# Kernel tuning notes

Measured on AMD Instinct MI355X. Metric: run time of the kernel, lower is better.

Reference implementation:

```python
import jax, jax.numpy as jnp
import numpy as np

N_NODES = 100000
N_EDGES = 1600000
NFEAT, NHID, NCLASS = 512, 128, 40


def setup_inputs() -> dict:
    key = jax.random.key(0)
    ks = jax.random.split(key, 8)
    features = jax.random.normal(ks[0], (N_NODES, NFEAT), dtype=jnp.float32)
    edge_src = jax.random.randint(ks[1], (N_EDGES,), 0, N_NODES, dtype=jnp.int32)
    edge_dst = jax.random.randint(ks[2], (N_EDGES,), 0, N_NODES, dtype=jnp.int32)
    edge_weight = jax.random.uniform(ks[3], (N_EDGES,), dtype=jnp.float32)
    W1 = jax.random.normal(ks[4], (NFEAT, NHID), dtype=jnp.float32) * (1.0 / np.sqrt(NFEAT))
    b1 = jnp.zeros((NHID,), dtype=jnp.float32)
    W2 = jax.random.normal(ks[5], (NHID, NCLASS), dtype=jnp.float32) * (1.0 / np.sqrt(NHID))
    b2 = jnp.zeros((NCLASS,), dtype=jnp.float32)
    return {"features": features, "edge_src": edge_src, "edge_dst": edge_dst,
            "edge_weight": edge_weight, "W1": W1, "b1": b1, "W2": W2, "b2": b2}


def _gcn_conv(x, W, b, edge_src, edge_dst, edge_weight, num_nodes):
    # GCNconv: adj @ (x @ W) + b, adj given as weighted edge list (spmm).
    h = x @ W                                   # [N, out]
    msgs = edge_weight[:, None] * h[edge_src]   # [E, out] gather + scale
    agg = jax.ops.segment_sum(msgs, edge_dst, num_segments=num_nodes)  # [N, out]
    return agg + b


def reference(features, edge_src, edge_dst, edge_weight, W1, b1, W2, b2):
    x = _gcn_conv(features, W1, b1, edge_src, edge_dst, edge_weight, N_NODES)
    x = jax.nn.relu(x)
    # dropout is identity in eval mode (deterministic reference)
    x = _gcn_conv(x, W2, b2, edge_src, edge_dst, edge_weight, N_NODES)
    return jax.nn.log_softmax(x, axis=1)
```

## Files before the change

kernel.cpp:

```cpp
#include <hip/hip_runtime.h>
#include <hip/hip_bf16.h>
#include <math.h>

#define N_NODES 100000
#define N_EDGES 1600000
#define NFEAT 512
#define NHID 128
#define NCLASS 40

#define SCAN_TILE 1024
#define SCAN_NB ((N_NODES + SCAN_TILE - 1) / SCAN_TILE)

#define BSH 8
#define BNODES (1 << BSH)
#define NBUCK ((N_NODES + BNODES - 1) / BNODES)

#define PCHUNK 4096
#define PEPT 16
#define PNB ((N_EDGES + PCHUNK - 1) / PCHUNK)

typedef short bf16x8 __attribute__((ext_vector_type(8)));
typedef float f32x4 __attribute__((ext_vector_type(4)));

static __device__ __forceinline__ unsigned short f32_to_bf16(float f) {
    unsigned int u = __float_as_uint(f);
    unsigned int r = u + 0x7FFFu + ((u >> 16) & 1u);
    return (unsigned short)(r >> 16);
}
static __device__ __forceinline__ float bf16_to_f32(unsigned short h) {
    return __uint_as_float(((unsigned int)h) << 16);
}

__global__ __launch_bounds__(256) void transpose_w1_kernel(
    const float* __restrict__ W1, unsigned short* __restrict__ Wt)
{
    int tid = blockIdx.x * 256 + threadIdx.x;
    int n = tid >> 9;
    int k = tid & 511;
    Wt[tid] = f32_to_bf16(W1[k * NHID + n]);
}

__global__ __launch_bounds__(256) void gemm1_mfma_kernel(
    const float* __restrict__ A,
    const unsigned short* __restrict__ Wt,
    unsigned short* __restrict__ h1b,
    int M)
{
    __shared__ unsigned short cstage[4][32 * 130];

    const int tid = threadIdx.x;
    const int w = tid >> 6;
    const int lane = tid & 63;
    const int lr = lane & 15;
    const int quad = lane >> 4;
    const int m0 = blockIdx.x * 128 + w * 32;

    f32x4 acc[2][8];
    #pragma unroll
    for (int rt = 0; rt < 2; rt++)
        #pragma unroll
        for (int ct = 0; ct < 8; ct++)
            acc[rt][ct] = (f32x4){0.f, 0.f, 0.f, 0.f};

    int r0 = m0 + lr;
    int r1 = m0 + 16 + lr;
    int r0c = r0 < M ? r0 : M - 1;
    int r1c = r1 < M ? r1 : M - 1;
    const float* a0p = A + (size_t)r0c * NFEAT + quad * 8;
    const float* a1p = A + (size_t)r1c * NFEAT + quad * 8;
    const unsigned short* bp = Wt + (size_t)lr * NFEAT + quad * 8;

    #pragma unroll 2
    for (int k0 = 0; k0 < NFEAT; k0 += 32) {
        float4 a0a = *(const float4*)(a0p + k0);
        float4 a0b = *(const float4*)(a0p + k0 + 4);
        float4 a1a = *(const float4*)(a1p + k0);
        float4 a1b = *(const float4*)(a1p + k0 + 4);

        bf16x8 fb[8];
        #pragma unroll
        for (int ct = 0; ct < 8; ct++)
            fb[ct] = *(const bf16x8*)(bp + (size_t)ct * 16 * NFEAT + k0);

        bf16x8 fa0, fa1;
        fa0[0] = (short)f32_to_bf16(a0a.x); fa0[1] = (short)f32_to_bf16(a0a.y);
        fa0[2] = (short)f32_to_bf16(a0a.z); fa0[3] = (short)f32_to_bf16(a0a.w);
        fa0[4] = (short)f32_to_bf16(a0b.x); fa0[5] = (short)f32_to_bf16(a0b.y);
        fa0[6] = (short)f32_to_bf16(a0b.z); fa0[7] = (short)f32_to_bf16(a0b.w);
        fa1[0] = (short)f32_to_bf16(a1a.x); fa1[1] = (short)f32_to_bf16(a1a.y);
        fa1[2] = (short)f32_to_bf16(a1a.z); fa1[3] = (short)f32_to_bf16(a1a.w);
        fa1[4] = (short)f32_to_bf16(a1b.x); fa1[5] = (short)f32_to_bf16(a1b.y);
        fa1[6] = (short)f32_to_bf16(a1b.z); fa1[7] = (short)f32_to_bf16(a1b.w);

        #pragma unroll
        for (int ct = 0; ct < 8; ct++) {
            acc[0][ct] = __builtin_amdgcn_mfma_f32_16x16x32_bf16(fa0, fb[ct], acc[0][ct], 0, 0, 0);
            acc[1][ct] = __builtin_amdgcn_mfma_f32_16x16x32_bf16(fa1, fb[ct], acc[1][ct], 0, 0, 0);
        }
    }

    unsigned short* st = cstage[w];
    #pragma unroll
    for (int rt = 0; rt < 2; rt++)
        #pragma unroll
        for (int ct = 0; ct < 8; ct++)
            #pragma unroll
            for (int i = 0; i < 4; i++) {
                int row = rt * 16 + quad * 4 + i;
                int col = ct * 16 + lr;
                st[row * 130 + col] = f32_to_bf16(acc[rt][ct][i]);
            }

    #pragma unroll
    for (int g = 0; g < 8; g++) {
        int row = g * 4 + (lane >> 4);
        int c8 = lane & 15;
        const unsigned short* rp = &st[row * 130 + c8 * 8];
        uint4 v = *(const uint4*)rp;
        int gr = m0 + row;
        if (gr < M)
            *(uint4*)&h1b[(size_t)gr * NHID + c8 * 8] = v;
    }
}

__global__ __launch_bounds__(256) void hist_kernel(
    const int* __restrict__ dst, int* __restrict__ counts, int E)
{
    int e = blockIdx.x * 256 + threadIdx.x;
    if (e < E) atomicAdd(&counts[dst[e]], 1);
}

__global__ __launch_bounds__(256) void scan_partials_kernel(
    const int* __restrict__ counts, int* __restrict__ partials, int N)
{
    __shared__ int sh[256];
    const int t = threadIdx.x;
    const int base = blockIdx.x * SCAN_TILE + t * 4;
    int s = 0;
    #pragma unroll
    for (int j = 0; j < 4; j++) {
        int i = base + j;
        if (i < N) s += counts[i];
    }
    sh[t] = s;
    __syncthreads();
    #pragma unroll
    for (int off = 128; off > 0; off >>= 1) {
        if (t < off) sh[t] += sh[t + off];
        __syncthreads();
    }
    if (t == 0) partials[blockIdx.x] = sh[0];
}

__global__ __launch_bounds__(128) void scan_offsets_kernel(
    const int* __restrict__ partials, int* __restrict__ bofs,
    int* __restrict__ offsets, int N)
{
    __shared__ int sh[128];
    const int t = threadIdx.x;
    int v = (t < SCAN_NB) ? partials[t] : 0;
    sh[t] = v;
    __syncthreads();
    #pragma unroll
    for (int off = 1; off < 128; off <<= 1) {
        int u = (t >= off) ? sh[t - off] : 0;
        __syncthreads();
        sh[t] += u;
        __syncthreads();
    }
    if (t < SCAN_NB) bofs[t] = sh[t] - v;
    if (t == 127) offsets[N] = sh[127];
}

__global__ __launch_bounds__(256) void scan_final_kernel(
    const int* __restrict__ counts, const int* __restrict__ bofs,
    int* __restrict__ offsets, int N)
{
    __shared__ int sh[256];
    const int t = threadIdx.x;
    const int base = blockIdx.x * SCAN_TILE + t * 4;
    int c[4] = {0, 0, 0, 0};
    #pragma unroll
    for (int j = 0; j < 4; j++) {
        int i = base + j;
        if (i < N) c[j] = counts[i];
    }
    int s = c[0] + c[1] + c[2] + c[3];
    sh[t] = s;
    __syncthreads();
    #pragma unroll
    for (int off = 1; off < 256; off <<= 1) {
        int u = (t >= off) ? sh[t - off] : 0;
        __syncthreads();
        sh[t] += u;
        __syncthreads();
    }
    int run = bofs[blockIdx.x] + sh[t] - s;
    #pragma unroll
    for (int j = 0; j < 4; j++) {
        int i = base + j;
        if (i < N) {
            offsets[i] = run;
            run += c[j];
        }
    }
}

__global__ __launch_bounds__(256) void bucket_init_kernel(
    const int* __restrict__ offsets, int* __restrict__ bcursor, int N)
{
    int b = blockIdx.x * 256 + threadIdx.x;
    if (b < NBUCK) {
        int nb = b << BSH;
        bcursor[b] = offsets[nb < N ? nb : N];
    }
}

__global__ __launch_bounds__(256) void partition_kernel(
    const int* __restrict__ src, const int* __restrict__ dst,
    const float* __restrict__ w, int* __restrict__ bcursor,
    int2* __restrict__ sortedA, int E)
{
    __shared__ int hist[NBUCK];
    __shared__ int bbase[NBUCK];
    const int t = threadIdx.x;
    const int c0 = blockIdx.x * PCHUNK;

    for (int j = t; j < NBUCK; j += 256) hist[j] = 0;
    __syncthreads();

    int  myb[PEPT];
    int2 myv[PEPT];
    #pragma unroll
    for (int i = 0; i < PEPT; i++) {
        int e = c0 + t + i * 256;
        if (e < E) {
            int d = dst[e];
            myb[i] = d >> BSH;
            myv[i] = make_int2(src[e] | ((d & (BNODES - 1)) << 17),
                               __float_as_int(w[e]));
            atomicAdd(&hist[myb[i]], 1);
        } else {
            myb[i] = -1;
        }
    }
    __syncthreads();

    for (int j = t; j < NBUCK; j += 256) {
        int c = hist[j];
        bbase[j] = c ? atomicAdd(&bcursor[j], c) : 0;
    }
    __syncthreads();

    #pragma unroll
    for (int i = 0; i < PEPT; i++) {
        if (myb[i] >= 0) {
            int p = atomicAdd(&bbase[myb[i]], 1);
            sortedA[p] = myv[i];
        }
    }
}

__global__ __launch_bounds__(256) void bucket_sort_kernel(
    const int2* __restrict__ sortedA, const int* __restrict__ offsets,
    int2* __restrict__ sortedB, int N)
{
    __shared__ int lcur[BNODES];
    const int b = blockIdx.x;
    const int t = threadIdx.x;
    const int nb = b << BSH;
    const int nn = min(BNODES, N - nb);
    if (t < nn) lcur[t] = offsets[nb + t];
    __syncthreads();
    const int beg = offsets[nb];
    const int end = offsets[nb + nn < N ? nb + nn : N];
    for (int e = beg + t; e < end; e += 256) {
        int2 v = sortedA[e];
        int dlow = (v.x >> 17) & (BNODES - 1);
        int s = v.x & 0x1FFFF;
        int p = atomicAdd(&lcur[dlow], 1);
        sortedB[p] = make_int2(s, v.y);
    }
}

__global__ __launch_bounds__(256) void seg_agg1_kernel(
    const int2* __restrict__ sorted, const int* __restrict__ offsets,
    const unsigned short* __restrict__ h1b, const float* __restrict__ b1,
    float* __restrict__ x, int N)
{
    const int tid = threadIdx.x;
    const int lane = tid & 31;
    const int node = blockIdx.x * 8 + (tid >> 5);
    if (node >= N) return;
    const int beg = offsets[node];
    const int end = offsets[node + 1];
    float4 acc = {0.f, 0.f, 0.f, 0.f};
    for (int c = beg; c < end; c += 32) {
        int m = end - c;
        if (m > 32) m = 32;
        int s = 0, wb = 0;
        if (lane < m) { int2 sw = sorted[c + lane]; s = sw.x; wb = sw.y; }
        for (int j = 0; j < m; j++) {
            int sj = __shfl(s, j, 32);
            float wj = __int_as_float(__shfl(wb, j, 32));
            ushort4 hv = *(const ushort4*)(h1b + (size_t)sj * NHID + lane * 4);
            acc.x = fmaf(wj, bf16_to_f32(hv.x), acc.x);
            acc.y = fmaf(wj, bf16_to_f32(hv.y), acc.y);
            acc.z = fmaf(wj, bf16_to_f32(hv.z), acc.z);
            acc.w = fmaf(wj, bf16_to_f32(hv.w), acc.w);
        }
    }
    float4 bb = *(const float4*)&b1[lane * 4];
    acc.x = fmaxf(acc.x + bb.x, 0.f);
    acc.y = fmaxf(acc.y + bb.y, 0.f);
    acc.z = fmaxf(acc.z + bb.z, 0.f);
    acc.w = fmaxf(acc.w + bb.w, 0.f);
    *(float4*)&x[(size_t)node * NHID + lane * 4] = acc;
}

__global__ __launch_bounds__(256) void gemm2_kernel(
    const float* __restrict__ x, const float* __restrict__ W2,
    float* __restrict__ h2, int M)
{
    __shared__ float xs[32][128];
    __shared__ float Wt[40][132];

    const int tid = threadIdx.x;
    const int m0 = blockIdx.x * 32;

    #pragma unroll
    for (int i = 0; i < 4; i++) {
        int v = tid + i * 256;
        int row = v >> 5;
        int c4 = (v & 31) * 4;
        *(float4*)&xs[row][c4] = *(const float4*)&x[(size_t)(m0 + row) * NHID + c4];
    }
    #pragma unroll
    for (int i = 0; i < 20; i++) {
        int v = tid + i * 256;
        int k = v / 40;
        int c = v - k * 40;
        Wt[c][k] = W2[v];
    }
    __syncthreads();

    #pragma unroll
    for (int i = 0; i < 5; i++) {
        int o = tid + i * 256;
        int row = o / 40;
        int col = o - row * 40;
        float s = 0.f;
        #pragma unroll
        for (int k4 = 0; k4 < 32; k4++) {
            float4 x4 = *(float4*)&xs[row][k4 * 4];
            float4 w4 = *(float4*)&Wt[col][k4 * 4];
            s = fmaf(x4.x, w4.x, s);
            s = fmaf(x4.y, w4.y, s);
            s = fmaf(x4.z, w4.z, s);
            s = fmaf(x4.w, w4.w, s);
        }
        h2[(size_t)(m0 + row) * NCLASS + col] = s;
    }
}

__global__ __launch_bounds__(256) void seg_agg2_kernel(
    const int2* __restrict__ sorted, const int* __restrict__ offsets,
    const float* __restrict__ h2, const float* __restrict__ b2,
    float* __restrict__ out, int N)
{
    const int tid = threadIdx.x;
    const int lane = tid & 15;
    const int node = blockIdx.x * 16 + (tid >> 4);
    if (node >= N) return;
    const int beg = offsets[node];
    const int end = offsets[node + 1];
    float4 acc = {0.f, 0.f, 0.f, 0.f};
    for (int c = beg; c < end; c += 16) {
        int m = end - c;
        if (m > 16) m = 16;
        int s = 0, wb = 0;
        if (lane < m) { int2 sw = sorted[c + lane]; s = sw.x; wb = sw.y; }
        for (int j = 0; j < m; j++) {
            int sj = __shfl(s, j, 16);
            float wj = __int_as_float(__shfl(wb, j, 16));
            if (lane < 10) {
                float4 v = *(const float4*)&h2[(size_t)sj * NCLASS + lane * 4];
                acc.x = fmaf(wj, v.x, acc.x);
                acc.y = fmaf(wj, v.y, acc.y);
                acc.z = fmaf(wj, v.z, acc.z);
                acc.w = fmaf(wj, v.w, acc.w);
            }
        }
    }
    float mx;
    if (lane < 10) {
        float4 bb = *(const float4*)&b2[lane * 4];
        acc.x += bb.x; acc.y += bb.y; acc.z += bb.z; acc.w += bb.w;
        mx = fmaxf(fmaxf(acc.x, acc.y), fmaxf(acc.z, acc.w));
    } else {
        mx = -INFINITY;
    }
    #pragma unroll
    for (int o = 8; o > 0; o >>= 1) mx = fmaxf(mx, __shfl_xor(mx, o, 16));
    float sm = 0.f;
    if (lane < 10)
        sm = expf(acc.x - mx) + expf(acc.y - mx) + expf(acc.z - mx) + expf(acc.w - mx);
    #pragma unroll
    for (int o = 8; o > 0; o >>= 1) sm += __shfl_xor(sm, o, 16);
    if (lane < 10) {
        float l = mx + logf(sm);
        float4 o4 = {acc.x - l, acc.y - l, acc.z - l, acc.w - l};
        *(float4*)&out[(size_t)node * NCLASS + lane * 4] = o4;
    }
}

extern "C" void kernel_launch(void* const* d_in, const int* in_sizes, int n_in,
                              void* d_out, int out_size, void* d_ws, size_t ws_size,
                              hipStream_t stream) {
    const float* features = (const float*)d_in[0];
    const int* edge_src   = (const int*)d_in[1];
    const int* edge_dst   = (const int*)d_in[2];
    const float* edge_w   = (const float*)d_in[3];
    const float* W1       = (const float*)d_in[4];
    const float* b1       = (const float*)d_in[5];
    const float* W2       = (const float*)d_in[6];
    const float* b2       = (const float*)d_in[7];
    float* out = (float*)d_out;

    char* base = (char*)d_ws;
    float*          x        = (float*)base;
    unsigned short* h1b      = (unsigned short*)(base + 51200000);
    unsigned short* Wt       = (unsigned short*)(base + 76800000);
    int2*           sortedB  = (int2*)(base + 76931072);
    int*            offsets  = (int*)(base + 89731072);
    int*            counts   = (int*)(base + 90131080);
    int*            partials = (int*)(base + 90531080);
    int*            bofs     = (int*)(base + 90531472);
    int*            bcursor  = (int*)(base + 90532000);
    int2*           sortedA  = (int2*)(base + 90540000);
    float*          h2       = (float*)h1b;

    hipMemsetAsync(counts, 0, N_NODES * sizeof(int), stream);

    hist_kernel<<<(N_EDGES + 255) / 256, 256, 0, stream>>>(edge_dst, counts, N_EDGES);
    scan_partials_kernel<<<SCAN_NB, 256, 0, stream>>>(counts, partials, N_NODES);
    scan_offsets_kernel<<<1, 128, 0, stream>>>(partials, bofs, offsets, N_NODES);
    scan_final_kernel<<<SCAN_NB, 256, 0, stream>>>(counts, bofs, offsets, N_NODES);
    bucket_init_kernel<<<(NBUCK + 255) / 256, 256, 0, stream>>>(offsets, bcursor, N_NODES);
    partition_kernel<<<PNB, 256, 0, stream>>>(
        edge_src, edge_dst, edge_w, bcursor, sortedA, N_EDGES);
    bucket_sort_kernel<<<NBUCK, 256, 0, stream>>>(sortedA, offsets, sortedB, N_NODES);

    transpose_w1_kernel<<<(NFEAT * NHID) / 256, 256, 0, stream>>>(W1, Wt);
    gemm1_mfma_kernel<<<(N_NODES + 127) / 128, 256, 0, stream>>>(features, Wt, h1b, N_NODES);

    seg_agg1_kernel<<<(N_NODES + 7) / 8, 256, 0, stream>>>(
        sortedB, offsets, h1b, b1, x, N_NODES);

    gemm2_kernel<<<(N_NODES + 31) / 32, 256, 0, stream>>>(x, W2, h2, N_NODES);

    seg_agg2_kernel<<<(N_NODES + 15) / 16, 256, 0, stream>>>(
        sortedB, offsets, h2, b2, out, N_NODES);
}
```

Measured before the change: 645.4 us.

## Replace per-node CSR sort with bucket partition and LDS-atomic aggregation fused with gemm2

Drops the full per-node histogram, three-pass scan and second-level bucket sort. Edges are now only partitioned into 128-node buckets. Each bucket block accumulates messages into shared memory with LDS float atomics, then fuses bias, ReLU and the second GEMM (layer 1), or bias and log-softmax (layer 2). The W1 transpose is folded into the histogram launch, removing several launches and a global round trip of the intermediate x. The cost is LDS atomic contention, nondeterministic summation order, and W2 rounded to bf16.

```diff
diff --git a/kernel.cpp b/kernel.cpp
--- a/kernel.cpp
+++ b/kernel.cpp
@@ -8,10 +8,7 @@
 #define NHID 128
 #define NCLASS 40
 
-#define SCAN_TILE 1024
-#define SCAN_NB ((N_NODES + SCAN_TILE - 1) / SCAN_TILE)
-
-#define BSH 8
+#define BSH 7
 #define BNODES (1 << BSH)
 #define NBUCK ((N_NODES + BNODES - 1) / BNODES)
 
@@ -31,189 +28,57 @@
     return __uint_as_float(((unsigned int)h) << 16);
 }
 
-__global__ __launch_bounds__(256) void transpose_w1_kernel(
-    const float* __restrict__ W1, unsigned short* __restrict__ Wt)
-{
-    int tid = blockIdx.x * 256 + threadIdx.x;
-    int n = tid >> 9;
-    int k = tid & 511;
-    Wt[tid] = f32_to_bf16(W1[k * NHID + n]);
-}
-
-__global__ __launch_bounds__(256) void gemm1_mfma_kernel(
-    const float* __restrict__ A,
-    const unsigned short* __restrict__ Wt,
-    unsigned short* __restrict__ h1b,
-    int M)
-{
-    __shared__ unsigned short cstage[4][32 * 130];
-
-    const int tid = threadIdx.x;
-    const int w = tid >> 6;
-    const int lane = tid & 63;
-    const int lr = lane & 15;
-    const int quad = lane >> 4;
-    const int m0 = blockIdx.x * 128 + w * 32;
-
-    f32x4 acc[2][8];
-    #pragma unroll
-    for (int rt = 0; rt < 2; rt++)
-        #pragma unroll
-        for (int ct = 0; ct < 8; ct++)
-            acc[rt][ct] = (f32x4){0.f, 0.f, 0.f, 0.f};
-
-    int r0 = m0 + lr;
-    int r1 = m0 + 16 + lr;
-    int r0c = r0 < M ? r0 : M - 1;
-    int r1c = r1 < M ? r1 : M - 1;
-    const float* a0p = A + (size_t)r0c * NFEAT + quad * 8;
-    const float* a1p = A + (size_t)r1c * NFEAT + quad * 8;
-    const unsigned short* bp = Wt + (size_t)lr * NFEAT + quad * 8;
-
-    #pragma unroll 2
-    for (int k0 = 0; k0 < NFEAT; k0 += 32) {
-        float4 a0a = *(const float4*)(a0p + k0);
-        float4 a0b = *(const float4*)(a0p + k0 + 4);
-        float4 a1a = *(const float4*)(a1p + k0);
-        float4 a1b = *(const float4*)(a1p + k0 + 4);
-
-        bf16x8 fb[8];
-        #pragma unroll
-        for (int ct = 0; ct < 8; ct++)
-            fb[ct] = *(const bf16x8*)(bp + (size_t)ct * 16 * NFEAT + k0);
-
-        bf16x8 fa0, fa1;
-        fa0[0] = (short)f32_to_bf16(a0a.x); fa0[1] = (short)f32_to_bf16(a0a.y);
-        fa0[2] = (short)f32_to_bf16(a0a.z); fa0[3] = (short)f32_to_bf16(a0a.w);
-        fa0[4] = (short)f32_to_bf16(a0b.x); fa0[5] = (short)f32_to_bf16(a0b.y);
-        fa0[6] = (short)f32_to_bf16(a0b.z); fa0[7] = (short)f32_to_bf16(a0b.w);
-        fa1[0] = (short)f32_to_bf16(a1a.x); fa1[1] = (short)f32_to_bf16(a1a.y);
-        fa1[2] = (short)f32_to_bf16(a1a.z); fa1[3] = (short)f32_to_bf16(a1a.w);
-        fa1[4] = (short)f32_to_bf16(a1b.x); fa1[5] = (short)f32_to_bf16(a1b.y);
-        fa1[6] = (short)f32_to_bf16(a1b.z); fa1[7] = (short)f32_to_bf16(a1b.w);
-
-        #pragma unroll
-        for (int ct = 0; ct < 8; ct++) {
-            acc[0][ct] = __builtin_amdgcn_mfma_f32_16x16x32_bf16(fa0, fb[ct], acc[0][ct], 0, 0, 0);
-            acc[1][ct] = __builtin_amdgcn_mfma_f32_16x16x32_bf16(fa1, fb[ct], acc[1][ct], 0, 0, 0);
-        }
-    }
-
-    unsigned short* st = cstage[w];
-    #pragma unroll
-    for (int rt = 0; rt < 2; rt++)
-        #pragma unroll
-        for (int ct = 0; ct < 8; ct++)
-            #pragma unroll
-            for (int i = 0; i < 4; i++) {
-                int row = rt * 16 + quad * 4 + i;
-                int col = ct * 16 + lr;
-                st[row * 130 + col] = f32_to_bf16(acc[rt][ct][i]);
-            }
-
-    #pragma unroll
-    for (int g = 0; g < 8; g++) {
-        int row = g * 4 + (lane >> 4);
-        int c8 = lane & 15;
-        const unsigned short* rp = &st[row * 130 + c8 * 8];
-        uint4 v = *(const uint4*)rp;
-        int gr = m0 + row;
-        if (gr < M)
-            *(uint4*)&h1b[(size_t)gr * NHID + c8 * 8] = v;
-    }
-}
-
-__global__ __launch_bounds__(256) void hist_kernel(
-    const int* __restrict__ dst, int* __restrict__ counts, int E)
-{
-    int e = blockIdx.x * 256 + threadIdx.x;
-    if (e < E) atomicAdd(&counts[dst[e]], 1);
-}
-
-__global__ __launch_bounds__(256) void scan_partials_kernel(
-    const int* __restrict__ counts, int* __restrict__ partials, int N)
-{
-    __shared__ int sh[256];
+__global__ __launch_bounds__(256) void bucket_hist_transpose_kernel(
+    const int* __restrict__ dst, int* __restrict__ histG,
+    const float* __restrict__ W1, unsigned short* __restrict__ Wt, int E)
+{
+    const int blk = blockIdx.x;
+    if (blk >= PNB) {
+        int tid2 = (blk - PNB) * 256 + threadIdx.x;
+        int n = tid2 >> 9;
+        int k = tid2 & 511;
+        Wt[tid2] = f32_to_bf16(W1[k * NHID + n]);
+        return;
+    }
+    __shared__ int hl[NBUCK];
     const int t = threadIdx.x;
-    const int base = blockIdx.x * SCAN_TILE + t * 4;
-    int s = 0;
-    #pragma unroll
-    for (int j = 0; j < 4; j++) {
-        int i = base + j;
-        if (i < N) s += counts[i];
-    }
-    sh[t] = s;
-    __syncthreads();
-    #pragma unroll
-    for (int off = 128; off > 0; off >>= 1) {
-        if (t < off) sh[t] += sh[t + off];
-        __syncthreads();
-    }
-    if (t == 0) partials[blockIdx.x] = sh[0];
-}
-
-__global__ __launch_bounds__(128) void scan_offsets_kernel(
-    const int* __restrict__ partials, int* __restrict__ bofs,
-    int* __restrict__ offsets, int N)
-{
-    __shared__ int sh[128];
+    for (int j = t; j < NBUCK; j += 256) hl[j] = 0;
+    __syncthreads();
+    const int c0 = blk * PCHUNK;
+    #pragma unroll
+    for (int i = 0; i < PEPT; i++) {
+        int e = c0 + t + i * 256;
+        if (e < E) atomicAdd(&hl[dst[e] >> BSH], 1);
+    }
+    __syncthreads();
+    for (int j = t; j < NBUCK; j += 256) {
+        int c = hl[j];
+        if (c) atomicAdd(&histG[j * 16], c);
+    }
+}
+
+__global__ __launch_bounds__(1024) void bucket_scan_kernel(
+    const int* __restrict__ histG, int* __restrict__ bofs,
+    int* __restrict__ bcursor)
+{
+    __shared__ int sh[1024];
     const int t = threadIdx.x;
-    int v = (t < SCAN_NB) ? partials[t] : 0;
+    int v = (t < NBUCK) ? histG[t * 16] : 0;
     sh[t] = v;
     __syncthreads();
     #pragma unroll
-    for (int off = 1; off < 128; off <<= 1) {
+    for (int off = 1; off < 1024; off <<= 1) {
         int u = (t >= off) ? sh[t - off] : 0;
         __syncthreads();
         sh[t] += u;
         __syncthreads();
     }
-    if (t < SCAN_NB) bofs[t] = sh[t] - v;
-    if (t == 127) offsets[N] = sh[127];
-}
-
-__global__ __launch_bounds__(256) void scan_final_kernel(
-    const int* __restrict__ counts, const int* __restrict__ bofs,
-    int* __restrict__ offsets, int N)
-{
-    __shared__ int sh[256];
-    const int t = threadIdx.x;
-    const int base = blockIdx.x * SCAN_TILE + t * 4;
-    int c[4] = {0, 0, 0, 0};
-    #pragma unroll
-    for (int j = 0; j < 4; j++) {
-        int i = base + j;
-        if (i < N) c[j] = counts[i];
-    }
-    int s = c[0] + c[1] + c[2] + c[3];
-    sh[t] = s;
-    __syncthreads();
-    #pragma unroll
-    for (int off = 1; off < 256; off <<= 1) {
-        int u = (t >= off) ? sh[t - off] : 0;
-        __syncthreads();
-        sh[t] += u;
-        __syncthreads();
-    }
-    int run = bofs[blockIdx.x] + sh[t] - s;
-    #pragma unroll
-    for (int j = 0; j < 4; j++) {
-        int i = base + j;
-        if (i < N) {
-            offsets[i] = run;
-            run += c[j];
-        }
-    }
-}
-
-__global__ __launch_bounds__(256) void bucket_init_kernel(
-    const int* __restrict__ offsets, int* __restrict__ bcursor, int N)
-{
-    int b = blockIdx.x * 256 + threadIdx.x;
-    if (b < NBUCK) {
-        int nb = b << BSH;
-        bcursor[b] = offsets[nb < N ? nb : N];
-    }
+    if (t < NBUCK) {
+        int excl = sh[t] - v;
+        bofs[t] = excl;
+        bcursor[t] = excl;
+    }
+    if (t == NBUCK - 1) bofs[NBUCK] = sh[t];
 }
 
 __global__ __launch_bounds__(256) void partition_kernel(
@@ -261,156 +126,256 @@
     }
 }
 
-__global__ __launch_bounds__(256) void bucket_sort_kernel(
-    const int2* __restrict__ sortedA, const int* __restrict__ offsets,
-    int2* __restrict__ sortedB, int N)
-{
-    __shared__ int lcur[BNODES];
+__global__ __launch_bounds__(256) void gemm1_mfma_kernel(
+    const float* __restrict__ A,
+    const unsigned short* __restrict__ Wt,
+    unsigned short* __restrict__ h1b,
+    int M)
+{
+    __shared__ unsigned short cstage[4][32 * 130];
+
+    const int tid = threadIdx.x;
+    const int w = tid >> 6;
+    const int lane = tid & 63;
+    const int lr = lane & 15;
+    const int quad = lane >> 4;
+    const int m0 = blockIdx.x * 128 + w * 32;
+
+    f32x4 acc[2][8];
+    #pragma unroll
+    for (int rt = 0; rt < 2; rt++)
+        #pragma unroll
+        for (int ct = 0; ct < 8; ct++)
+            acc[rt][ct] = (f32x4){0.f, 0.f, 0.f, 0.f};
+
+    int r0 = m0 + lr;
+    int r1 = m0 + 16 + lr;
+    int r0c = r0 < M ? r0 : M - 1;
+    int r1c = r1 < M ? r1 : M - 1;
+    const float* a0p = A + (size_t)r0c * NFEAT + quad * 8;
+    const float* a1p = A + (size_t)r1c * NFEAT + quad * 8;
+    const unsigned short* bp = Wt + (size_t)lr * NFEAT + quad * 8;
+
+    #pragma unroll 2
+    for (int k0 = 0; k0 < NFEAT; k0 += 32) {
+        float4 a0a = *(const float4*)(a0p + k0);
+        float4 a0b = *(const float4*)(a0p + k0 + 4);
+        float4 a1a = *(const float4*)(a1p + k0);
+        float4 a1b = *(const float4*)(a1p + k0 + 4);
+
+        bf16x8 fb[8];
+        #pragma unroll
+        for (int ct = 0; ct < 8; ct++)
+            fb[ct] = *(const bf16x8*)(bp + (size_t)ct * 16 * NFEAT + k0);
+
+        bf16x8 fa0, fa1;
+        fa0[0] = (short)f32_to_bf16(a0a.x); fa0[1] = (short)f32_to_bf16(a0a.y);
+        fa0[2] = (short)f32_to_bf16(a0a.z); fa0[3] = (short)f32_to_bf16(a0a.w);
+        fa0[4] = (short)f32_to_bf16(a0b.x); fa0[5] = (short)f32_to_bf16(a0b.y);
+        fa0[6] = (short)f32_to_bf16(a0b.z); fa0[7] = (short)f32_to_bf16(a0b.w);
+        fa1[0] = (short)f32_to_bf16(a1a.x); fa1[1] = (short)f32_to_bf16(a1a.y);
+        fa1[2] = (short)f32_to_bf16(a1a.z); fa1[3] = (short)f32_to_bf16(a1a.w);
+        fa1[4] = (short)f32_to_bf16(a1b.x); fa1[5] = (short)f32_to_bf16(a1b.y);
+        fa1[6] = (short)f32_to_bf16(a1b.z); fa1[7] = (short)f32_to_bf16(a1b.w);
+
+        #pragma unroll
+        for (int ct = 0; ct < 8; ct++) {
+            acc[0][ct] = __builtin_amdgcn_mfma_f32_16x16x32_bf16(fa0, fb[ct], acc[0][ct], 0, 0, 0);
+            acc[1][ct] = __builtin_amdgcn_mfma_f32_16x16x32_bf16(fa1, fb[ct], acc[1][ct], 0, 0, 0);
+        }
+    }
+
+    unsigned short* st = cstage[w];
+    #pragma unroll
+    for (int rt = 0; rt < 2; rt++)
+        #pragma unroll
+        for (int ct = 0; ct < 8; ct++)
+            #pragma unroll
+            for (int i = 0; i < 4; i++) {
+                int row = rt * 16 + quad * 4 + i;
+                int col = ct * 16 + lr;
+                st[row * 130 + col] = f32_to_bf16(acc[rt][ct][i]);
+            }
+
+    #pragma unroll
+    for (int g = 0; g < 8; g++) {
+        int row = g * 4 + (lane >> 4);
+        int c8 = lane & 15;
+        const unsigned short* rp = &st[row * 130 + c8 * 8];
+        uint4 v = *(const uint4*)rp;
+        int gr = m0 + row;
+        if (gr < M)
+            *(uint4*)&h1b[(size_t)gr * NHID + c8 * 8] = v;
+    }
+}
+
+__global__ __launch_bounds__(256) void agg1_gemm2_kernel(
+    const int2* __restrict__ sortedA, const int* __restrict__ bofs,
+    const unsigned short* __restrict__ h1b, const float* __restrict__ b1,
+    const float* __restrict__ W2, float* __restrict__ h2, int N)
+{
+    __shared__ __align__(16) float accf[128 * 132];
+    __shared__ __align__(16) unsigned short wt2[40 * 132];
+    __shared__ float b1p[128];
+
+    const int tid = threadIdx.x;
     const int b = blockIdx.x;
-    const int t = threadIdx.x;
-    const int nb = b << BSH;
-    const int nn = min(BNODES, N - nb);
-    if (t < nn) lcur[t] = offsets[nb + t];
-    __syncthreads();
-    const int beg = offsets[nb];
-    const int end = offsets[nb + nn < N ? nb + nn : N];
-    for (int e = beg + t; e < end; e += 256) {
-        int2 v = sortedA[e];
-        int dlow = (v.x >> 17) & (BNODES - 1);
-        int s = v.x & 0x1FFFF;
-        int p = atomicAdd(&lcur[dlow], 1);
-        sortedB[p] = make_int2(s, v.y);
-    }
-}
-
-__global__ __launch_bounds__(256) void seg_agg1_kernel(
-    const int2* __restrict__ sorted, const int* __restrict__ offsets,
-    const unsigned short* __restrict__ h1b, const float* __restrict__ b1,
-    float* __restrict__ x, int N)
-{
-    const int tid = threadIdx.x;
-    const int lane = tid & 31;
-    const int node = blockIdx.x * 8 + (tid >> 5);
-    if (node >= N) return;
-    const int beg = offsets[node];
-    const int end = offsets[node + 1];
-    float4 acc = {0.f, 0.f, 0.f, 0.f};
-    for (int c = beg; c < end; c += 32) {
-        int m = end - c;
-        if (m > 32) m = 32;
-        int s = 0, wb = 0;
-        if (lane < m) { int2 sw = sorted[c + lane]; s = sw.x; wb = sw.y; }
-        for (int j = 0; j < m; j++) {
-            int sj = __shfl(s, j, 32);
-            float wj = __int_as_float(__shfl(wb, j, 32));
-            ushort4 hv = *(const ushort4*)(h1b + (size_t)sj * NHID + lane * 4);
-            acc.x = fmaf(wj, bf16_to_f32(hv.x), acc.x);
-            acc.y = fmaf(wj, bf16_to_f32(hv.y), acc.y);
-            acc.z = fmaf(wj, bf16_to_f32(hv.z), acc.z);
-            acc.w = fmaf(wj, bf16_to_f32(hv.w), acc.w);
-        }
-    }
-    float4 bb = *(const float4*)&b1[lane * 4];
-    acc.x = fmaxf(acc.x + bb.x, 0.f);
-    acc.y = fmaxf(acc.y + bb.y, 0.f);
-    acc.z = fmaxf(acc.z + bb.z, 0.f);
-    acc.w = fmaxf(acc.w + bb.w, 0.f);
-    *(float4*)&x[(size_t)node * NHID + lane * 4] = acc;
-}
-
-__global__ __launch_bounds__(256) void gemm2_kernel(
-    const float* __restrict__ x, const float* __restrict__ W2,
-    float* __restrict__ h2, int M)
-{
-    __shared__ float xs[32][128];
-    __shared__ float Wt[40][132];
-
-    const int tid = threadIdx.x;
-    const int m0 = blockIdx.x * 32;
-
-    #pragma unroll
-    for (int i = 0; i < 4; i++) {
-        int v = tid + i * 256;
-        int row = v >> 5;
-        int c4 = (v & 31) * 4;
-        *(float4*)&xs[row][c4] = *(const float4*)&x[(size_t)(m0 + row) * NHID + c4];
-    }
-    #pragma unroll
-    for (int i = 0; i < 20; i++) {
-        int v = tid + i * 256;
-        int k = v / 40;
-        int c = v - k * 40;
-        Wt[c][k] = W2[v];
-    }
-    __syncthreads();
-
-    #pragma unroll
-    for (int i = 0; i < 5; i++) {
-        int o = tid + i * 256;
-        int row = o / 40;
-        int col = o - row * 40;
+    const int node0 = b << BSH;
+    const int nn = min(BNODES, N - node0);
+
+    for (int i = tid; i < 128 * 132; i += 256) accf[i] = 0.f;
+    for (int i = tid; i < 40 * 128; i += 256) {
+        int c = i >> 7;
+        int w = i & 127;
+        int d = ((w & 63) << 1) | (w >> 6);
+        wt2[c * 132 + w] = f32_to_bf16(W2[d * NCLASS + c]);
+    }
+    if (tid < 128) {
+        int d = ((tid & 63) << 1) | (tid >> 6);
+        b1p[tid] = b1[d];
+    }
+    __syncthreads();
+
+    const int beg = bofs[b];
+    const int end = bofs[b + 1];
+    const int wv = tid >> 6;
+    const int lane = tid & 63;
+
+    for (int base = beg + wv * 64; base < end; base += 256) {
+        const int cnt = min(64, end - base);
+        int rx = 0, ry = 0;
+        if (lane < cnt) { int2 r = sortedA[base + lane]; rx = r.x; ry = r.y; }
+        for (int j0 = 0; j0 < cnt; j0 += 8) {
+            const int g = min(8, cnt - j0);
+            int xs_[8]; float ws_[8];
+            #pragma unroll
+            for (int q = 0; q < 8; q++) {
+                xs_[q] = __shfl(rx, j0 + q, 64);
+                ws_[q] = __int_as_float(__shfl(ry, j0 + q, 64));
+            }
+            unsigned int vv[8];
+            #pragma unroll
+            for (int q = 0; q < 8; q++) {
+                if (q < g) {
+                    const unsigned int* rp =
+                        (const unsigned int*)(h1b + (size_t)(xs_[q] & 0x1FFFF) * NHID);
+                    vv[q] = rp[lane];
+                }
+            }
+            #pragma unroll
+            for (int q = 0; q < 8; q++) {
+                if (q < g) {
+                    float* ar = &accf[((xs_[q] >> 17) & 127) * 132];
+                    float lo = bf16_to_f32((unsigned short)(vv[q] & 0xFFFF));
+                    float hi = bf16_to_f32((unsigned short)(vv[q] >> 16));
+                    unsafeAtomicAdd(&ar[lane], ws_[q] * lo);
+                    unsafeAtomicAdd(&ar[64 + lane], ws_[q] * hi);
+                }
+            }
+        }
+    }
+    __syncthreads();
+
+    for (int i = tid; i < (nn << 7); i += 256) {
+        int r = i >> 7, w = i & 127;
+        int idx = r * 132 + w;
+        accf[idx] = fmaxf(accf[idx] + b1p[w], 0.f);
+    }
+    __syncthreads();
+
+    float* hp = h2 + (size_t)node0 * NCLASS;
+    for (int o = tid; o < nn * NCLASS; o += 256) {
+        int r = o / NCLASS;
+        int c = o - r * NCLASS;
+        const float* ap = &accf[r * 132];
+        const unsigned short* wp = &wt2[c * 132];
         float s = 0.f;
         #pragma unroll
-        for (int k4 = 0; k4 < 32; k4++) {
-            float4 x4 = *(float4*)&xs[row][k4 * 4];
-            float4 w4 = *(float4*)&Wt[col][k4 * 4];
-            s = fmaf(x4.x, w4.x, s);
-            s = fmaf(x4.y, w4.y, s);
-            s = fmaf(x4.z, w4.z, s);
-            s = fmaf(x4.w, w4.w, s);
-        }
-        h2[(size_t)(m0 + row) * NCLASS + col] = s;
-    }
-}
-
-__global__ __launch_bounds__(256) void seg_agg2_kernel(
-    const int2* __restrict__ sorted, const int* __restrict__ offsets,
+        for (int k = 0; k < 128; k += 4) {
+            float4 a4 = *(const float4*)(ap + k);
+            ushort4 w4 = *(const ushort4*)(wp + k);
+            s = fmaf(a4.x, bf16_to_f32(w4.x), s);
+            s = fmaf(a4.y, bf16_to_f32(w4.y), s);
+            s = fmaf(a4.z, bf16_to_f32(w4.z), s);
+            s = fmaf(a4.w, bf16_to_f32(w4.w), s);
+        }
+        hp[o] = s;
+    }
+}
+
+__global__ __launch_bounds__(256) void agg2_softmax_kernel(
+    const int2* __restrict__ sortedA, const int* __restrict__ bofs,
     const float* __restrict__ h2, const float* __restrict__ b2,
     float* __restrict__ out, int N)
 {
+    __shared__ __align__(16) float acc2[128 * 40];
+
     const int tid = threadIdx.x;
-    const int lane = tid & 15;
-    const int node = blockIdx.x * 16 + (tid >> 4);
-    if (node >= N) return;
-    const int beg = offsets[node];
-    const int end = offsets[node + 1];
-    float4 acc = {0.f, 0.f, 0.f, 0.f};
-    for (int c = beg; c < end; c += 16) {
-        int m = end - c;
-        if (m > 16) m = 16;
-        int s = 0, wb = 0;
-        if (lane < m) { int2 sw = sorted[c + lane]; s = sw.x; wb = sw.y; }
-        for (int j = 0; j < m; j++) {
-            int sj = __shfl(s, j, 16);
-            float wj = __int_as_float(__shfl(wb, j, 16));
-            if (lane < 10) {
-                float4 v = *(const float4*)&h2[(size_t)sj * NCLASS + lane * 4];
-                acc.x = fmaf(wj, v.x, acc.x);
-                acc.y = fmaf(wj, v.y, acc.y);
-                acc.z = fmaf(wj, v.z, acc.z);
-                acc.w = fmaf(wj, v.w, acc.w);
-            }
-        }
-    }
-    float mx;
-    if (lane < 10) {
-        float4 bb = *(const float4*)&b2[lane * 4];
-        acc.x += bb.x; acc.y += bb.y; acc.z += bb.z; acc.w += bb.w;
-        mx = fmaxf(fmaxf(acc.x, acc.y), fmaxf(acc.z, acc.w));
-    } else {
-        mx = -INFINITY;
-    }
-    #pragma unroll
-    for (int o = 8; o > 0; o >>= 1) mx = fmaxf(mx, __shfl_xor(mx, o, 16));
-    float sm = 0.f;
-    if (lane < 10)
-        sm = expf(acc.x - mx) + expf(acc.y - mx) + expf(acc.z - mx) + expf(acc.w - mx);
-    #pragma unroll
-    for (int o = 8; o > 0; o >>= 1) sm += __shfl_xor(sm, o, 16);
-    if (lane < 10) {
-        float l = mx + logf(sm);
-        float4 o4 = {acc.x - l, acc.y - l, acc.z - l, acc.w - l};
-        *(float4*)&out[(size_t)node * NCLASS + lane * 4] = o4;
+    const int b = blockIdx.x;
+    const int node0 = b << BSH;
+    const int nn = min(BNODES, N - node0);
+
+    for (int i = tid; i < 128 * 40; i += 256) acc2[i] = 0.f;
+    __syncthreads();
+
+    const int beg = bofs[b];
+    const int end = bofs[b + 1];
+    const int wv = tid >> 6;
+    const int lane = tid & 63;
+
+    for (int base = beg + wv * 64; base < end; base += 256) {
+        const int cnt = min(64, end - base);
+        int rx = 0, ry = 0;
+        if (lane < cnt) { int2 r = sortedA[base + lane]; rx = r.x; ry = r.y; }
+        for (int j0 = 0; j0 < cnt; j0 += 8) {
+            const int g = min(8, cnt - j0);
+            int xs_[8]; float ws_[8];
+            #pragma unroll
+            for (int q = 0; q < 8; q++) {
+                xs_[q] = __shfl(rx, j0 + q, 64);
+                ws_[q] = __int_as_float(__shfl(ry, j0 + q, 64));
+            }
+            float vv[8];
+            #pragma unroll
+            for (int q = 0; q < 8; q++) {
+                if (q < g && lane < NCLASS)
+                    vv[q] = h2[(size_t)(xs_[q] & 0x1FFFF) * NCLASS + lane];
+            }
+            #pragma unroll
+            for (int q = 0; q < 8; q++) {
+                if (q < g && lane < NCLASS)
+                    unsafeAtomicAdd(&acc2[((xs_[q] >> 17) & 127) * NCLASS + lane],
+                                    ws_[q] * vv[q]);
+            }
+        }
+    }
+    __syncthreads();
+
+    const int l16 = tid & 15;
+    const int grp = tid >> 4;
+    #pragma unroll
+    for (int it = 0; it < 8; it++) {
+        int ln = grp + (it << 4);
+        bool act = (ln < nn) && (l16 < 10);
+        float4 a = {0.f, 0.f, 0.f, 0.f};
+        float mx = -INFINITY;
+        if (act) {
+            a = *(const float4*)&acc2[ln * NCLASS + l16 * 4];
+            float4 bb = *(const float4*)&b2[l16 * 4];
+            a.x += bb.x; a.y += bb.y; a.z += bb.z; a.w += bb.w;
+            mx = fmaxf(fmaxf(a.x, a.y), fmaxf(a.z, a.w));
+        }
+        #pragma unroll
+        for (int o = 8; o > 0; o >>= 1) mx = fmaxf(mx, __shfl_xor(mx, o, 16));
+        float sm = act ? expf(a.x - mx) + expf(a.y - mx) +
+                         expf(a.z - mx) + expf(a.w - mx) : 0.f;
+        #pragma unroll
+        for (int o = 8; o > 0; o >>= 1) sm += __shfl_xor(sm, o, 16);
+        if (act) {
+            float l = mx + logf(sm);
+            float4 o4 = {a.x - l, a.y - l, a.z - l, a.w - l};
+            *(float4*)&out[(size_t)(node0 + ln) * NCLASS + l16 * 4] = o4;
+        }
     }
 }
 
@@ -428,37 +393,27 @@
     float* out = (float*)d_out;
 
     char* base = (char*)d_ws;
-    float*          x        = (float*)base;
+    float*          h2       = (float*)base;
     unsigned short* h1b      = (unsigned short*)(base + 51200000);
     unsigned short* Wt       = (unsigned short*)(base + 76800000);
-    int2*           sortedB  = (int2*)(base + 76931072);
-    int*            offsets  = (int*)(base + 89731072);
-    int*            counts   = (int*)(base + 90131080);
-    int*            partials = (int*)(base + 90531080);
-    int*            bofs     = (int*)(base + 90531472);
-    int*            bcursor  = (int*)(base + 90532000);
+    int*            histG    = (int*)(base + 76931072);
+    int*            bofs     = (int*)(base + 77000000);
+    int*            bcursor  = (int*)(base + 77010000);
     int2*           sortedA  = (int2*)(base + 90540000);
-    float*          h2       = (float*)h1b;
-
-    hipMemsetAsync(counts, 0, N_NODES * sizeof(int), stream);
-
-    hist_kernel<<<(N_EDGES + 255) / 256, 256, 0, stream>>>(edge_dst, counts, N_EDGES);
-    scan_partials_kernel<<<SCAN_NB, 256, 0, stream>>>(counts, partials, N_NODES);
-    scan_offsets_kernel<<<1, 128, 0, stream>>>(partials, bofs, offsets, N_NODES);
-    scan_final_kernel<<<SCAN_NB, 256, 0, stream>>>(counts, bofs, offsets, N_NODES);
-    bucket_init_kernel<<<(NBUCK + 255) / 256, 256, 0, stream>>>(offsets, bcursor, N_NODES);
+
+    hipMemsetAsync(histG, 0, NBUCK * 16 * sizeof(int), stream);
+
+    bucket_hist_transpose_kernel<<<PNB + (NFEAT * NHID) / 256, 256, 0, stream>>>(
+        edge_dst, histG, W1, Wt, N_EDGES);
+    bucket_scan_kernel<<<1, 1024, 0, stream>>>(histG, bofs, bcursor);
     partition_kernel<<<PNB, 256, 0, stream>>>(
         edge_src, edge_dst, edge_w, bcursor, sortedA, N_EDGES);
-    bucket_sort_kernel<<<NBUCK, 256, 0, stream>>>(sortedA, offsets, sortedB, N_NODES);
-
-    transpose_w1_kernel<<<(NFEAT * NHID) / 256, 256, 0, stream>>>(W1, Wt);
+
     gemm1_mfma_kernel<<<(N_NODES + 127) / 128, 256, 0, stream>>>(features, Wt, h1b, N_NODES);
 
-    seg_agg1_kernel<<<(N_NODES + 7) / 8, 256, 0, stream>>>(
-        sortedB, offsets, h1b, b1, x, N_NODES);
-
-    gemm2_kernel<<<(N_NODES + 31) / 32, 256, 0, stream>>>(x, W2, h2, N_NODES);
-
-    seg_agg2_kernel<<<(N_NODES + 15) / 16, 256, 0, stream>>>(
-        sortedB, offsets, h2, b2, out, N_NODES);
-}
+    agg1_gemm2_kernel<<<NBUCK, 256, 0, stream>>>(
+        sortedA, bofs, h1b, b1, W2, h2, N_NODES);
+
+    agg2_softmax_kernel<<<NBUCK, 256, 0, stream>>>(
+        sortedA, bofs, h2, b2, out, N_NODES);
+}
```

After: 2.362 ms. +266.0%, slower.
